# Optimization experiments

Measured on AMD Instinct MI355X. Metric: run time of the kernel, lower is better.

Reference implementation:

```python
import math
import jax, jax.numpy as jnp
import numpy as np

B, S, DIM = 2, 4096, 512
HEADS, DIM_HEAD, CHUNK = 8, 64, 64
DIM_INNER = HEADS * DIM_HEAD
EPS = 1e-6


def rmsnorm(x, scale):
    var = jnp.mean(x * x, axis=-1, keepdims=True)
    return x * jax.lax.rsqrt(var + EPS) * scale


def mem_attn(p, x):
    # x: [c, dh] single chunk; tiny causal attention memory model
    q = x @ p['wq']
    k = x @ p['wk']
    v = x @ p['wv1']
    d = q.shape[-1]
    dots = (q @ k.T) * (d ** -0.5)
    c = x.shape[-2]
    mask = jnp.tril(jnp.ones((c, c), dtype=bool))
    dots = jnp.where(mask, dots, -1e9)
    attn = jax.nn.softmax(dots, axis=-1)
    hidden = attn @ v
    return jax.nn.silu(hidden) @ p['wv2']


def mem_loss(p, inp, tgt):
    pred = mem_attn(p, inp)
    return jnp.sum(jnp.mean((pred - tgt) ** 2, axis=-1))


def assoc_scan(gates, vals):
    # first-order linear recurrence y_t = g_t * y_{t-1} + v_t along axis=1
    def op(a, b):
        a1, b1 = a
        a2, b2 = b
        return a1 * a2, a2 * b1 + b2
    return jax.lax.associative_scan(op, (gates, vals), axis=1)


def setup_inputs():
    key = jax.random.key(0)
    ks = jax.random.split(key, 16)
    n = lambda k, shp, s: jax.random.normal(k, shp, dtype=jnp.float32) * s
    return {
        'seq': n(ks[0], (B, S, DIM), 1.0),
        'w_store_norm': jnp.ones((DIM,), jnp.float32),
        'w_retrieve_norm': jnp.ones((DIM,), jnp.float32),
        'w_post_norm': jnp.ones((DIM,), jnp.float32),
        'w_q': n(ks[1], (DIM, DIM_INNER), DIM ** -0.5),
        'w_kv': n(ks[2], (DIM, 2 * DIM_INNER), DIM ** -0.5),
        'w_step': n(ks[3], (DIM, HEADS), DIM ** -0.5),
        'w_mom': n(ks[4], (DIM, HEADS), DIM ** -0.5),
        'w_decay': n(ks[5], (DIM, HEADS), DIM ** -0.5),
        'w_combine': n(ks[6], (DIM_INNER, DIM), DIM_INNER ** -0.5),
        'wq': n(ks[7], (DIM_HEAD, DIM_HEAD), 0.01),
        'wk': n(ks[8], (DIM_HEAD, DIM_HEAD), 0.01),
        'wv1': n(ks[9], (DIM_HEAD, DIM_HEAD), 0.01),
        'wv2': n(ks[10], (DIM_HEAD, DIM_HEAD), 0.01),
    }


def reference(seq, w_store_norm, w_retrieve_norm, w_post_norm, w_q, w_kv,
              w_step, w_mom, w_decay, w_combine, wq, wk, wv1, wv2):
    b, s_len, d = seq.shape
    c, h, dh = CHUNK, HEADS, DIM_HEAD
    past = {'wq': wq, 'wk': wk, 'wv1': wv1, 'wv2': wv2}

    # ---------- store_memories ----------
    s = rmsnorm(seq, w_store_norm)
    n_full = (s_len // c) * c
    s = s[:, :n_full]
    nc = n_full // c

    # adaptive lr: [b,n,h] -> (b h) n -> chunk-mean [bh, nc]
    lr = jnp.exp(jax.nn.sigmoid(s @ w_step) * -15.0)
    lr = jnp.transpose(lr, (0, 2, 1)).reshape(b * h, nc, c).mean(-1)

    s_mean = s.reshape(b, nc, c, d).mean(2)  # [b, nc, d]
    mom_gate = jax.nn.sigmoid(s_mean @ w_mom)
    mom_gate = jnp.transpose(mom_gate, (0, 2, 1)).reshape(b * h, nc, 1)
    decay = jax.nn.sigmoid(s_mean @ w_decay)
    decay = jnp.transpose(decay, (0, 2, 1)).reshape(b * h, nc, 1)

    keys, values = jnp.split(s @ w_kv, 2, axis=-1)

    def chunkify(t):  # [b, n, h*dh] -> [(b h nc), c, dh]
        t = t.reshape(b, n_full, h, dh)
        t = jnp.transpose(t, (0, 2, 1, 3))
        return t.reshape(b * h * nc, c, dh)

    keys, values = chunkify(keys), chunkify(values)

    # per-chunk meta-gradients wrt shared memory-model params
    grads = jax.vmap(jax.grad(mem_loss), in_axes=(None, 0, 0))(past, keys, values)

    updates = {}
    for name in past:
        g = grads[name].reshape(b * h, nc, dh * dh)
        surprise = g * (-lr)[..., None]
        _, momentum = assoc_scan(mom_gate, surprise)
        _, upd = assoc_scan(1.0 - decay, momentum)
        updates[name] = upd.reshape(b * h, nc, dh, dh)

    wwu = {k2: past[k2][None, None] + updates[k2] for k2 in past}  # [bh, nc, dh, dh]

    # ---------- retrieve_memories ----------
    r = rmsnorm(seq, w_retrieve_norm)
    rc = r[:, c:]
    curtailed = s_len - c
    next_len = ((curtailed + 1 + c - 1) // c) * c
    pad = next_len - curtailed
    rc = jnp.pad(rc, ((0, 0), (0, pad), (0, 0)))

    q = rc @ w_q  # [b, next_len, h*dh]
    q = q.reshape(b, next_len, h, dh)
    q = jnp.transpose(q, (0, 2, 1, 3)).reshape(b * h * (next_len // c), c, dh)

    pc = {k2: v2.reshape(b * h * nc, dh, dh) for k2, v2 in wwu.items()}
    vals = jax.vmap(mem_attn)(pc, q)  # [(bh nc), c, dh]
    vals = vals.reshape(b, h, next_len, dh)
    vals = jnp.transpose(vals, (0, 2, 1, 3)).reshape(b, next_len, h * dh)
    vals = rmsnorm(vals @ w_combine, w_post_norm)
    vals = jnp.pad(vals, ((0, 0), (c, 0), (0, 0)))
    return vals[:, :-pad]
```

## Files before the change

kernel.cpp:

```cpp
#include <hip/hip_runtime.h>
#include <math.h>

constexpr int BATCH = 2, SEQ = 4096, DIM = 512, HEADS = 8, DH = 64, CH = 64;
constexpr int NC = SEQ / CH;
constexpr int BH = BATCH * HEADS;
constexpr int NCHUNK = BH * NC;
constexpr int ROWS = BATCH * SEQ;
constexpr int DI = HEADS * DH;
constexpr int TS = 64 * 72;

typedef __attribute__((ext_vector_type(8))) short short8;
typedef __attribute__((ext_vector_type(4))) short short4v;
typedef __attribute__((ext_vector_type(4))) float f32x4;

__device__ inline float sigmoidf_(float x){ return 1.f/(1.f+__expf(-x)); }
__device__ inline float dsilu_f(float x){ float s = sigmoidf_(x); return s*(1.f + x*(1.f-s)); }

__device__ inline unsigned short f2b(float f){
  union { float f; unsigned int u; } c; c.f = f;
  unsigned int u = c.u;
  unsigned int r = (u + 0x7FFFu + ((u >> 16) & 1u)) >> 16;
  return (unsigned short)r;
}
__device__ inline float b2f(unsigned short h){
  union { unsigned int u; float f; } c; c.u = ((unsigned int)h) << 16;
  return c.f;
}

struct MM { int lr, lg, rowbase, colbase; };
__device__ inline MM mmctx(){
  int tid = threadIdx.x;
  int wid = tid >> 6, lane = tid & 63;
  MM m; m.lr = lane & 15; m.lg = lane >> 4;
  m.rowbase = (wid >> 1) * 16; m.colbase = (wid & 1) * 32;
  return m;
}

template<bool SILUA>
__device__ inline void mm64(const unsigned short* A, const unsigned short* B,
                            f32x4 (&acc)[2], const MM& m)
{
  acc[0] = (f32x4){0.f,0.f,0.f,0.f};
  acc[1] = (f32x4){0.f,0.f,0.f,0.f};
  #pragma unroll
  for (int ks = 0; ks < 2; ks++){
    short8 a = *(const short8*)&A[(m.rowbase + m.lr)*72 + ks*32 + m.lg*8];
    if constexpr (SILUA){
      #pragma unroll
      for (int j = 0; j < 8; j++){
        float v = b2f((unsigned short)a[j]);
        v = v * sigmoidf_(v);
        a[j] = (short)f2b(v);
      }
    }
    #pragma unroll
    for (int ct = 0; ct < 2; ct++){
      short8 b = *(const short8*)&B[(m.colbase + ct*16 + m.lr)*72 + ks*32 + m.lg*8];
      acc[ct] = __builtin_amdgcn_mfma_f32_16x16x32_bf16(a, b, acc[ct], 0, 0, 0);
    }
  }
}

__device__ inline void storeN64(unsigned short* R, const f32x4 (&acc)[2], const MM& m, float scale){
  #pragma unroll
  for (int ct = 0; ct < 2; ct++){
    int c  = m.colbase + ct*16 + m.lr;
    int mb = m.rowbase + m.lg*4;
    #pragma unroll
    for (int r = 0; r < 4; r++) R[(mb+r)*72 + c] = f2b(acc[ct][r] * scale);
  }
}
__device__ inline void storeT64(unsigned short* T, const f32x4 (&acc)[2], const MM& m, float scale){
  #pragma unroll
  for (int ct = 0; ct < 2; ct++){
    int c  = m.colbase + ct*16 + m.lr;
    int mb = m.rowbase + m.lg*4;
    short4v p;
    #pragma unroll
    for (int r = 0; r < 4; r++) p[r] = (short)f2b(acc[ct][r] * scale);
    *(short4v*)&T[c*72 + mb] = p;
  }
}
__device__ inline void storeSC(float* S, const f32x4 (&acc)[2], const MM& m, float scale){
  #pragma unroll
  for (int ct = 0; ct < 2; ct++){
    int c  = m.colbase + ct*16 + m.lr;
    int mb = m.rowbase + m.lg*4;
    #pragma unroll
    for (int r = 0; r < 4; r++) S[(mb+r)*66 + c] = acc[ct][r] * scale;
  }
}
__device__ inline void storeGTb64(unsigned short* __restrict__ G, const f32x4 (&acc)[2],
                                  const MM& m, float scale){
  #pragma unroll
  for (int ct = 0; ct < 2; ct++){
    int c  = m.colbase + ct*16 + m.lr;
    int mb = m.rowbase + m.lg*4;
    short4v p;
    #pragma unroll
    for (int r = 0; r < 4; r++) p[r] = (short)f2b(acc[ct][r] * scale);
    *(short4v*)&G[c*64 + mb] = p;
  }
}

__device__ inline void loadTileBrow(unsigned short* R, const unsigned short* __restrict__ src,
                                    int stride, int tid){
  int i = tid >> 3, j8 = (tid & 7) * 8;
  *(short8*)&R[i*72 + j8] = *(const short8*)&src[(size_t)i*stride + j8];
}
__device__ inline void loadTileBrowT(unsigned short* R, unsigned short* T,
                                     const unsigned short* __restrict__ src,
                                     int stride, int tid){
  int i = tid >> 3, j8 = (tid & 7) * 8;
  short8 v = *(const short8*)&src[(size_t)i*stride + j8];
  *(short8*)&R[i*72 + j8] = v;
  #pragma unroll
  for (int jj = 0; jj < 8; jj++) T[(j8+jj)*72 + i] = (unsigned short)v[jj];
}

__global__ __launch_bounds__(256) void k_front(
    const float* __restrict__ seq, const float* __restrict__ wsn,
    const float* __restrict__ wrn, const float* __restrict__ wstep,
    const float* __restrict__ w_kv, const float* __restrict__ w_q,
    const float* __restrict__ wcomb,
    const float* __restrict__ wq, const float* __restrict__ wk,
    const float* __restrict__ wv1, const float* __restrict__ wv2,
    unsigned short* __restrict__ s_hi, unsigned short* __restrict__ s_lo,
    unsigned short* __restrict__ rq_hi, float* __restrict__ lrp,
    unsigned short* __restrict__ wkvT_hi, unsigned short* __restrict__ wkvT_lo,
    unsigned short* __restrict__ wqT_hi, unsigned short* __restrict__ wcombT_hi,
    unsigned short* __restrict__ wpre)
{
  __shared__ float t[64][65];
  int tid = threadIdx.x;
  if (blockIdx.x >= ROWS/4){
    int blk = blockIdx.x - ROWS/4;
    if (blk < 256){
      const float* src; unsigned short *dhi, *dlo;
      int R, C, bx, by;
      if (blk < 128){ src = w_kv;  dhi = wkvT_hi;  dlo = wkvT_lo; R = DIM; C = 2*DI; bx = blk & 15; by = blk >> 4; }
      else if (blk < 192){ int q = blk - 128; src = w_q;   dhi = wqT_hi;    dlo = nullptr; R = DIM; C = DI;  bx = q & 7; by = q >> 3; }
      else               { int q = blk - 192; src = wcomb; dhi = wcombT_hi; dlo = nullptr; R = DI;  C = DIM; bx = q & 7; by = q >> 3; }
      int c0 = bx * 64, r0 = by * 64;
      #pragma unroll
      for (int it = 0; it < 16; it++){
        int idx = it*256 + tid;
        int i = idx >> 6, j = idx & 63;
        t[i][j] = src[(size_t)(r0+i)*C + c0 + j];
      }
      __syncthreads();
      #pragma unroll
      for (int it = 0; it < 16; it++){
        int idx = it*256 + tid;
        int i = idx >> 6, j = idx & 63;
        float v = t[j][i];
        unsigned short hi = f2b(v);
        dhi[(size_t)(c0+i)*R + r0 + j] = hi;
        if (dlo) dlo[(size_t)(c0+i)*R + r0 + j] = f2b(v - b2f(hi));
      }
    } else {
      int b = blk - 256;
      const float* src = (b==0) ? wq : (b==1) ? wk : (b==2) ? wv1 : wv2;
      #pragma unroll
      for (int it = 0; it < 16; it++){
        int idx = it*256 + tid;
        int i = idx >> 6, j = idx & 63;
        t[i][j] = src[i*64 + j];
      }
      __syncthreads();
      #pragma unroll
      for (int it = 0; it < 16; it++){
        int idx = it*256 + tid;
        int i = idx >> 6, j = idx & 63;
        wpre[b*4096 + i*64 + j] = f2b(t[j][i]);
        if (b == 3) wpre[4*4096 + i*64 + j] = f2b(t[i][j]);
      }
    }
    return;
  }
  int wid = tid >> 6, lane = tid & 63;
  int row = blockIdx.x * 4 + wid;
  int b = row >> 12, tt = row & 4095;
  const float* x = seq + (size_t)row * DIM;
  float4 v0 = *(const float4*)&x[lane*4];
  float4 v1 = *(const float4*)&x[256 + lane*4];
  float xv[8] = {v0.x, v0.y, v0.z, v0.w, v1.x, v1.y, v1.z, v1.w};
  float ss = 0.f;
  #pragma unroll
  for (int j = 0; j < 8; j++) ss += xv[j]*xv[j];
  #pragma unroll
  for (int m = 1; m < 64; m <<= 1) ss += __shfl_xor(ss, m);
  float rinv = rsqrtf(ss * (1.f/DIM) + 1e-6f);

  float4 w0 = *(const float4*)&wsn[lane*4];
  float4 w1 = *(const float4*)&wsn[256 + lane*4];
  float wv[8] = {w0.x, w0.y, w0.z, w0.w, w1.x, w1.y, w1.z, w1.w};
  float sv[8];
  short4v h0, h1, l0, l1;
  #pragma unroll
  for (int j = 0; j < 8; j++){
    sv[j] = xv[j] * rinv * wv[j];
    unsigned short hi = f2b(sv[j]);
    unsigned short lo = f2b(sv[j] - b2f(hi));
    if (j < 4){ h0[j] = (short)hi; l0[j] = (short)lo; }
    else      { h1[j-4] = (short)hi; l1[j-4] = (short)lo; }
  }
  size_t sbase = (size_t)row*DIM + lane*4;
  *(short4v*)&s_hi[sbase] = h0; *(short4v*)&s_hi[sbase + 256] = h1;
  *(short4v*)&s_lo[sbase] = l0; *(short4v*)&s_lo[sbase + 256] = l1;

  if (tt >= CH){
    float4 r0 = *(const float4*)&wrn[lane*4];
    float4 r1 = *(const float4*)&wrn[256 + lane*4];
    float rv[8] = {r0.x, r0.y, r0.z, r0.w, r1.x, r1.y, r1.z, r1.w};
    short4v rh0, rh1;
    #pragma unroll
    for (int j = 0; j < 8; j++){
      float q = xv[j] * rinv * rv[j];
      unsigned short hi = f2b(q);
      if (j < 4) rh0[j] = (short)hi; else rh1[j-4] = (short)hi;
    }
    size_t rbase = ((size_t)b*SEQ + (tt - CH))*DIM + lane*4;
    *(short4v*)&rq_hi[rbase] = rh0; *(short4v*)&rq_hi[rbase + 256] = rh1;
  } else {
    short4v z; z[0]=0; z[1]=0; z[2]=0; z[3]=0;
    size_t rbase = ((size_t)b*SEQ + (SEQ - CH + tt))*DIM + lane*4;
    *(short4v*)&rq_hi[rbase] = z; *(short4v*)&rq_hi[rbase + 256] = z;
  }

  float acc[8] = {0.f,0.f,0.f,0.f,0.f,0.f,0.f,0.f};
  #pragma unroll
  for (int j = 0; j < 8; j++){
    int e = (j < 4) ? (lane*4 + j) : (256 + lane*4 + (j-4));
    float4 wa = *(const float4*)&wstep[e*8];
    float4 wb = *(const float4*)&wstep[e*8 + 4];
    acc[0] += sv[j]*wa.x; acc[1] += sv[j]*wa.y; acc[2] += sv[j]*wa.z; acc[3] += sv[j]*wa.w;
    acc[4] += sv[j]*wb.x; acc[5] += sv[j]*wb.y; acc[6] += sv[j]*wb.z; acc[7] += sv[j]*wb.w;
  }
  #pragma unroll
  for (int m = 1; m < 64; m <<= 1){
    #pragma unroll
    for (int h = 0; h < 8; h++) acc[h] += __shfl_xor(acc[h], m);
  }
  float a = acc[0];
  #pragma unroll
  for (int h = 1; h < 8; h++) a = (lane == h) ? acc[h] : a;
  if (lane < 8)
    lrp[(size_t)row*HEADS + lane] = __expf(-15.f * sigmoidf_(a));
}

__global__ __launch_bounds__(256, 2) void k_mid(
    const unsigned short* __restrict__ s_hi, const unsigned short* __restrict__ s_lo,
    const unsigned short* __restrict__ rq_hi,
    const unsigned short* __restrict__ wkvT_hi, const unsigned short* __restrict__ wkvT_lo,
    const unsigned short* __restrict__ wqT_hi,
    unsigned short* __restrict__ kvb, unsigned short* __restrict__ qb,
    float* __restrict__ kvv,
    const float* __restrict__ lrp, const float* __restrict__ wmom,
    const float* __restrict__ wdec,
    float* __restrict__ mg, float* __restrict__ dec, float* __restrict__ lrc)
{
  __shared__ __align__(16) unsigned short AhS[128*72];
  __shared__ __align__(16) unsigned short BhS[128*72];
  __shared__ __align__(16) unsigned short AlS[128*72];
  __shared__ __align__(16) unsigned short BlS[128*72];
  int tid = threadIdx.x;
  int z = blockIdx.z;
  if (z == 3){
    int bid = blockIdx.y * gridDim.x + blockIdx.x;
    if (bid >= BATCH*NC) return;
    float* smean = (float*)AhS;
    int b = bid >> 6, ch = bid & 63;
    size_t off = ((size_t)(b*SEQ + ch*CH)) * DIM;
    for (int e = tid; e < DIM; e += 256){
      float acc = 0.f;
      for (int i = 0; i < CH; i++)
        acc += b2f(s_hi[off + (size_t)i*DIM + e]);
      smean[e] = acc * (1.f/CH);
    }
    __syncthreads();
    int gh = tid >> 5, l = tid & 31;
    float am = 0.f, ad = 0.f;
    for (int e = l; e < DIM; e += 32){
      float v = smean[e];
      am += v * wmom[e*HEADS + gh];
      ad += v * wdec[e*HEADS + gh];
    }
    const float* lrbase = lrp + ((size_t)(b*SEQ + ch*CH)) * HEADS + gh;
    float al = lrbase[(size_t)l*HEADS] + lrbase[(size_t)(l+32)*HEADS];
    #pragma unroll
    for (int m = 1; m < 32; m <<= 1){
      am += __shfl_xor(am, m);
      ad += __shfl_xor(ad, m);
      al += __shfl_xor(al, m);
    }
    if (l == 0){
      int o = (b*HEADS + gh)*NC + ch;
      mg[o]  = sigmoidf_(am);
      dec[o] = sigmoidf_(ad);
      lrc[o] = al * (1.f/CH);
    }
    return;
  }
  const bool LO = (z == 2);
  const unsigned short* Ahg = (z == 1) ? rq_hi : s_hi;
  const unsigned short* Alg = s_lo;
  const unsigned short* Bhg = (z == 0) ? wkvT_hi : (z == 1) ? wqT_hi
                                       : wkvT_hi + (size_t)DI*DIM;
  const unsigned short* Blg = wkvT_lo + (size_t)DI*DIM;
  const int M = ROWS, N = DI, K = DIM;

  int nwg = gridDim.x * gridDim.y;
  int bid = blockIdx.y * gridDim.x + blockIdx.x;
  int swz = (bid & 7) * (nwg >> 3) + (bid >> 3);
  int m0 = (swz / gridDim.x) * 128;
  int n0 = (swz % gridDim.x) * 128;
  int wid = tid >> 6, lane = tid & 63;
  int lr = lane & 15, lg = lane >> 4;
  int wr = (wid >> 1) * 64, wc = (wid & 1) * 64;
  f32x4 acc[4][4];
  #pragma unroll
  for (int r = 0; r < 4; r++)
    #pragma unroll
    for (int c = 0; c < 4; c++) acc[r][c] = (f32x4){0.f,0.f,0.f,0.f};

  for (int k0 = 0; k0 < K; k0 += 64){
    #pragma unroll
    for (int it = 0; it < 4; it++){
      int idx = it*256 + tid;
      int row = idx >> 3, col8 = (idx & 7) * 8;
      size_t ga = (size_t)(m0+row)*K + k0 + col8;
      size_t gb = (size_t)(n0+row)*K + k0 + col8;
      *(short8*)&AhS[row*72 + col8] = *(const short8*)&Ahg[ga];
      *(short8*)&BhS[row*72 + col8] = *(const short8*)&Bhg[gb];
      if (LO){
        *(short8*)&AlS[row*72 + col8] = *(const short8*)&Alg[ga];
        *(short8*)&BlS[row*72 + col8] = *(const short8*)&Blg[gb];
      }
    }
    __syncthreads();
    #pragma unroll
    for (int ks = 0; ks < 2; ks++){
      short8 ah[4], al[4], bh[4], bl[4];
      #pragma unroll
      for (int i = 0; i < 4; i++){
        int ao = (wr + i*16 + lr)*72 + ks*32 + lg*8;
        int bo = (wc + i*16 + lr)*72 + ks*32 + lg*8;
        ah[i] = *(const short8*)&AhS[ao];
        bh[i] = *(const short8*)&BhS[bo];
        if (LO){
          al[i] = *(const short8*)&AlS[ao];
          bl[i] = *(const short8*)&BlS[bo];
        }
      }
      #pragma unroll
      for (int r = 0; r < 4; r++)
        #pragma unroll
        for (int c = 0; c < 4; c++){
          acc[r][c] = __builtin_amdgcn_mfma_f32_16x16x32_bf16(ah[r], bh[c], acc[r][c], 0, 0, 0);
          if (LO){
            acc[r][c] = __builtin_amdgcn_mfma_f32_16x16x32_bf16(ah[r], bl[c], acc[r][c], 0, 0, 0);
            acc[r][c] = __builtin_amdgcn_mfma_f32_16x16x32_bf16(al[r], bh[c], acc[r][c], 0, 0, 0);
          }
        }
    }
    __syncthreads();
  }
  unsigned short* Cb = (z == 1) ? qb : kvb;
  #pragma unroll
  for (int rt = 0; rt < 4; rt++)
    #pragma unroll
    for (int ct = 0; ct < 4; ct++){
      int col = n0 + wc + ct*16 + lr;
      int rowb = m0 + wr + rt*16 + lg*4;
      #pragma unroll
      for (int r = 0; r < 4; r++){
        float v = acc[rt][ct][r];
        if (LO) kvv[(size_t)(rowb+r)*N + col] = v;
        else    Cb[(size_t)(rowb+r)*N + col] = f2b(v);
      }
    }
}

__global__ __launch_bounds__(256, 4) void k_gemm1(
    const unsigned short* __restrict__ Ahg, const unsigned short* __restrict__ Bhg,
    unsigned short* __restrict__ Cb, int M, int N, int K)
{
  __shared__ __align__(16) unsigned short AhS[128*72];
  __shared__ __align__(16) unsigned short BhS[128*72];
  int tid = threadIdx.x;
  int nwg = gridDim.x * gridDim.y;
  int bid = blockIdx.y * gridDim.x + blockIdx.x;
  int swz = (bid & 7) * (nwg >> 3) + (bid >> 3);
  int m0 = (swz / gridDim.x) * 128;
  int n0 = (swz % gridDim.x) * 128;
  int wid = tid >> 6, lane = tid & 63;
  int lr = lane & 15, lg = lane >> 4;
  int wr = (wid >> 1) * 64, wc = (wid & 1) * 64;
  f32x4 acc[4][4];
  #pragma unroll
  for (int r = 0; r < 4; r++)
    #pragma unroll
    for (int c = 0; c < 4; c++) acc[r][c] = (f32x4){0.f,0.f,0.f,0.f};

  for (int k0 = 0; k0 < K; k0 += 64){
    #pragma unroll
    for (int it = 0; it < 4; it++){
      int idx = it*256 + tid;
      int row = idx >> 3, col8 = (idx & 7) * 8;
      *(short8*)&AhS[row*72 + col8] = *(const short8*)&Ahg[(size_t)(m0+row)*K + k0 + col8];
      *(short8*)&BhS[row*72 + col8] = *(const short8*)&Bhg[(size_t)(n0+row)*K + k0 + col8];
    }
    __syncthreads();
    #pragma unroll
    for (int ks = 0; ks < 2; ks++){
      short8 ah[4], bh[4];
      #pragma unroll
      for (int i = 0; i < 4; i++){
        ah[i] = *(const short8*)&AhS[(wr + i*16 + lr)*72 + ks*32 + lg*8];
        bh[i] = *(const short8*)&BhS[(wc + i*16 + lr)*72 + ks*32 + lg*8];
      }
      #pragma unroll
      for (int r = 0; r < 4; r++)
        #pragma unroll
        for (int c = 0; c < 4; c++)
          acc[r][c] = __builtin_amdgcn_mfma_f32_16x16x32_bf16(ah[r], bh[c], acc[r][c], 0, 0, 0);
    }
    __syncthreads();
  }
  #pragma unroll
  for (int rt = 0; rt < 4; rt++)
    #pragma unroll
    for (int ct = 0; ct < 4; ct++){
      int col = n0 + wc + ct*16 + lr;
      int rowb = m0 + wr + rt*16 + lg*4;
      #pragma unroll
      for (int r = 0; r < 4; r++)
        Cb[(size_t)(rowb+r)*N + col] = f2b(acc[rt][ct][r]);
    }
}

__global__ __launch_bounds__(512) void k_grads(
    const unsigned short* __restrict__ kvb, const float* __restrict__ kvv,
    const unsigned short* __restrict__ wpre,
    const float* __restrict__ lrc, unsigned short* __restrict__ g)
{
  __shared__ __align__(16) unsigned short sm[12*TS];
  __shared__ __align__(16) float SC[64*66];
  unsigned short *Xr = sm,        *XT = sm + TS,
                 *s2 = sm + 2*TS, *s3 = sm + 3*TS, *s4 = sm + 4*TS,
                 *s5 = sm + 5*TS, *s6 = sm + 6*TS, *s7 = sm + 7*TS,
                 *s8 = sm + 8*TS, *s9 = sm + 9*TS, *s10 = sm + 10*TS,
                 *s11 = sm + 11*TS;
  unsigned short *SCu = (unsigned short*)SC;
  int chunk = blockIdx.x;
  int bh = chunk >> 6, t = chunk & 63;
  int b = bh >> 3, h = bh & 7;
  int tid = threadIdx.x;
  MM M = mmctx();
  const unsigned short* xb = kvb + ((size_t)(b*SEQ + t*CH)) * DI + h*DH;
  const float* tbase = kvv + ((size_t)(b*SEQ + t*CH)) * DI + h*DH;
  float negLr = -lrc[bh*NC + t];
  f32x4 acc[2], accV[2];

  loadTileBrowT(Xr, XT, xb, DI, tid);
  loadTileBrow(s2, wpre + 0*4096, 64, tid);
  loadTileBrow(s3, wpre + 1*4096, 64, tid);
  loadTileBrow(s4, wpre + 2*4096, 64, tid);
  loadTileBrow(s5, wpre + 3*4096, 64, tid);
  loadTileBrow(s6, wpre + 4*4096, 64, tid);
  __syncthreads();
  mm64<false>(Xr, s2, acc, M);
  storeN64(s7, acc, M, 1.f); storeT64(s8, acc, M, 1.f);
  mm64<false>(Xr, s3, acc, M);
  storeN64(s9, acc, M, 1.f); storeT64(s10, acc, M, 1.f);
  mm64<false>(Xr, s4, accV, M);
  storeN64(s11, accV, M, 1.f);
  __syncthreads();
  storeT64(s2, accV, M, 1.f);
  mm64<false>(s7, s9, acc, M);
  storeSC(SC, acc, M, 0.125f);
  __syncthreads();
  {
    int row = tid >> 3, q = tid & 7;
    float p[8];
    float mx = -1e30f;
    #pragma unroll
    for (int cc = 0; cc < 8; cc++){
      int col = q*8 + cc;
      float x = SC[row*66 + col];
      p[cc] = (col <= row) ? x : -1e9f;
      mx = fmaxf(mx, p[cc]);
    }
    mx = fmaxf(mx, __shfl_xor(mx, 1));
    mx = fmaxf(mx, __shfl_xor(mx, 2));
    mx = fmaxf(mx, __shfl_xor(mx, 4));
    float sum = 0.f;
    #pragma unroll
    for (int cc = 0; cc < 8; cc++){ p[cc] = __expf(p[cc] - mx); sum += p[cc]; }
    sum += __shfl_xor(sum, 1);
    sum += __shfl_xor(sum, 2);
    sum += __shfl_xor(sum, 4);
    float inv = 1.f / sum;
    #pragma unroll
    for (int cc = 0; cc < 8; cc++){
      int col = q*8 + cc;
      unsigned short hh = f2b(p[cc] * inv);
      s7[row*72 + col] = hh;
      s9[col*72 + row] = hh;
    }
  }
  __syncthreads();
  mm64<false>(s7, s2, acc, M);
  storeN64(s3, acc, M, 1.f); storeT64(s4, acc, M, 1.f);
  __syncthreads();
  mm64<true>(s3, s5, acc, M);
  #pragma unroll
  for (int ct = 0; ct < 2; ct++){
    int c  = M.colbase + ct*16 + M.lr;
    int mb = M.rowbase + M.lg*4;
    #pragma unroll
    for (int r = 0; r < 4; r++){
      float t2 = (acc[ct][r] - tbase[(size_t)(mb+r)*DI + c]) * (2.f/64.f);
      unsigned short hh = f2b(t2);
      Xr[(mb+r)*72 + c] = hh;
      s2[c*72 + (mb+r)] = hh;
    }
  }
  __syncthreads();
  mm64<true>(s4, s2, acc, M);
  storeGTb64(g + ((size_t)(3*NCHUNK + chunk))*4096, acc, M, negLr);
  mm64<false>(Xr, s6, acc, M);
  #pragma unroll
  for (int ct = 0; ct < 2; ct++){
    int c  = M.colbase + ct*16 + M.lr;
    int mb = M.rowbase + M.lg*4;
    #pragma unroll
    for (int r = 0; r < 4; r++){
      float x = b2f(s3[(mb+r)*72 + c]);
      float d = acc[ct][r] * dsilu_f(x);
      unsigned short hh = f2b(d);
      s5[(mb+r)*72 + c] = hh;
      SCu[c*72 + (mb+r)] = hh;
    }
  }
  __syncthreads();
  mm64<false>(s5, s11, acc, M);
  storeN64(Xr, acc, M, 1.f);
  mm64<false>(s9, SCu, acc, M);
  storeT64(s2, acc, M, 1.f);
  __syncthreads();
  {
    int row = tid >> 3, q = tid & 7;
    float da[8], a[8], rs = 0.f;
    #pragma unroll
    for (int cc = 0; cc < 8; cc++){
      int col = q*8 + cc;
      da[cc] = b2f(Xr[row*72 + col]);
      a[cc]  = b2f(s7[row*72 + col]);
      rs += da[cc]*a[cc];
    }
    rs += __shfl_xor(rs, 1);
    rs += __shfl_xor(rs, 2);
    rs += __shfl_xor(rs, 4);
    #pragma unroll
    for (int cc = 0; cc < 8; cc++){
      int col = q*8 + cc;
      unsigned short hh = f2b(a[cc] * (da[cc] - rs));
      s3[row*72 + col] = hh;
      s6[col*72 + row] = hh;
    }
  }
  mm64<false>(XT, s2, acc, M);
  storeGTb64(g + ((size_t)(2*NCHUNK + chunk))*4096, acc, M, negLr);
  __syncthreads();
  mm64<false>(s3, s10, acc, M);
  storeT64(Xr, acc, M, 0.125f);
  mm64<false>(s6, s8, acc, M);
  storeT64(s2, acc, M, 0.125f);
  __syncthreads();
  mm64<false>(XT, Xr, acc, M);
  storeGTb64(g + ((size_t)(0*NCHUNK + chunk))*4096, acc, M, negLr);
  mm64<false>(XT, s2, acc, M);
  storeGTb64(g + ((size_t)(1*NCHUNK + chunk))*4096, acc, M, negLr);
}

__global__ __launch_bounds__(256) void k_scan(
    unsigned short* __restrict__ g, const float* __restrict__ mg, const float* __restrict__ dec,
    const float* __restrict__ wq, const float* __restrict__ wk,
    const float* __restrict__ wv1, const float* __restrict__ wv2)
{
  int idx = blockIdx.x * 256 + threadIdx.x;
  int e = (idx & 2047) * 2;
  int bh = (idx >> 11) & 15;
  int name = idx >> 15;
  const float* past = (name == 0) ? wq : (name == 1) ? wk : (name == 2) ? wv1 : wv2;
  float base0 = past[(e & 63)*64 + (e >> 6)];
  float base1 = past[((e+1) & 63)*64 + ((e+1) >> 6)];
  const float* mgb = mg + bh*NC;
  const float* dcb = dec + bh*NC;
  size_t baseoff = ((size_t)name*NCHUNK + (size_t)bh*NC)*4096 + e;
  float m0 = 0.f, u0 = 0.f, m1 = 0.f, u1 = 0.f;
  for (int t = 0; t < NC; t++){
    size_t off = baseoff + (size_t)t*4096;
    unsigned int v = *(const unsigned int*)&g[off];
    float su0 = b2f((unsigned short)(v & 0xffff));
    float su1 = b2f((unsigned short)(v >> 16));
    float gm = mgb[t], dc = dcb[t];
    m0 = gm*m0 + su0;  u0 = (1.f - dc)*u0 + m0;
    m1 = gm*m1 + su1;  u1 = (1.f - dc)*u1 + m1;
    unsigned int w = (unsigned int)f2b(base0 + u0) | ((unsigned int)f2b(base1 + u1) << 16);
    *(unsigned int*)&g[off] = w;
  }
}

__global__ __launch_bounds__(512, 4) void k_retrieve(
    const unsigned short* __restrict__ qb, const unsigned short* __restrict__ Wg,
    unsigned short* __restrict__ vals_hi)
{
  __shared__ __align__(16) unsigned short sm[6*TS];
  __shared__ __align__(16) float SC[64*66];
  unsigned short *Xr = sm,       *Wt = sm + TS,   *Qr = sm + 2*TS,
                 *Kr = sm + 3*TS, *Vt = sm + 4*TS, *Hr = sm + 5*TS;
  unsigned short *Ar = (unsigned short*)SC;
  int chunk = blockIdx.x;
  int bh = chunk >> 6, t = chunk & 63;
  int b = bh >> 3, h = bh & 7;
  int tid = threadIdx.x;
  MM M = mmctx();
  const unsigned short* xb = qb + ((size_t)(b*SEQ + t*CH)) * DI + h*DH;
  f32x4 acc[2], accV[2];

  loadTileBrow(Xr, xb, DI, tid);
  loadTileBrow(Wt, Wg + ((size_t)(0*NCHUNK + chunk))*4096, 64, tid);
  __syncthreads();
  mm64<false>(Xr, Wt, acc, M); storeN64(Qr, acc, M, 1.f);
  loadTileBrow(Hr, Wg + ((size_t)(1*NCHUNK + chunk))*4096, 64, tid);
  __syncthreads();
  mm64<false>(Xr, Hr, acc, M); storeN64(Kr, acc, M, 1.f);
  loadTileBrow(Wt, Wg + ((size_t)(2*NCHUNK + chunk))*4096, 64, tid);
  __syncthreads();
  mm64<false>(Xr, Wt, accV, M); storeT64(Vt, accV, M, 1.f);
  mm64<false>(Qr, Kr, acc, M); storeSC(SC, acc, M, 0.125f);
  loadTileBrow(Hr, Wg + ((size_t)(3*NCHUNK + chunk))*4096, 64, tid);
  __syncthreads();
  {
    int row = tid >> 3, q = tid & 7;
    float p[8];
    float mx = -1e30f;
    #pragma unroll
    for (int cc = 0; cc < 8; cc++){
      int col = q*8 + cc;
      float x = SC[row*66 + col];
      p[cc] = (col <= row) ? x : -1e9f;
      mx = fmaxf(mx, p[cc]);
    }
    mx = fmaxf(mx, __shfl_xor(mx, 1));
    mx = fmaxf(mx, __shfl_xor(mx, 2));
    mx = fmaxf(mx, __shfl_xor(mx, 4));
    float sum = 0.f;
    #pragma unroll
    for (int cc = 0; cc < 8; cc++){ p[cc] = __expf(p[cc] - mx); sum += p[cc]; }
    sum += __shfl_xor(sum, 1);
    sum += __shfl_xor(sum, 2);
    sum += __shfl_xor(sum, 4);
    float inv = 1.f / sum;
    __syncthreads();
    #pragma unroll
    for (int cc = 0; cc < 8; cc++){
      int col = q*8 + cc;
      Ar[row*72 + col] = f2b(p[cc] * inv);
    }
  }
  __syncthreads();
  mm64<false>(Ar, Vt, acc, M); storeN64(Kr, acc, M, 1.f);
  __syncthreads();
  mm64<true>(Kr, Hr, acc, M);
  #pragma unroll
  for (int ct = 0; ct < 2; ct++){
    int c  = M.colbase + ct*16 + M.lr;
    int mb = M.rowbase + M.lg*4;
    #pragma unroll
    for (int r = 0; r < 4; r++){
      size_t o = ((size_t)(b*SEQ + t*CH + mb + r))*DI + h*DH + c;
      vals_hi[o] = f2b(acc[ct][r]);
    }
  }
}

__global__ __launch_bounds__(256) void k_outnorm(
    const unsigned short* __restrict__ tmp, const float* __restrict__ wpn,
    float* __restrict__ out)
{
  int wid = threadIdx.x >> 6, lane = threadIdx.x & 63;
  int row = blockIdx.x * 4 + wid;
  int b = row >> 12, r = row & 4095;
  float* dst = out + ((size_t)b*SEQ + r) * DIM;
  if (r < CH){
    float4 z = make_float4(0.f, 0.f, 0.f, 0.f);
    *(float4*)&dst[lane*8] = z;
    *(float4*)&dst[lane*8 + 4] = z;
    return;
  }
  const unsigned short* src = tmp + ((size_t)b*SEQ + (r - CH)) * DIM;
  short8 t0 = *(const short8*)&src[lane*8];
  float xv[8];
  #pragma unroll
  for (int j = 0; j < 8; j++) xv[j] = b2f((unsigned short)t0[j]);
  float ss = 0.f;
  #pragma unroll
  for (int j = 0; j < 8; j++) ss += xv[j]*xv[j];
  #pragma unroll
  for (int m = 1; m < 64; m <<= 1) ss += __shfl_xor(ss, m);
  float rinv = rsqrtf(ss * (1.f/DIM) + 1e-6f);
  float4 o0, o1;
  o0.x = xv[0]*rinv*wpn[lane*8+0]; o0.y = xv[1]*rinv*wpn[lane*8+1];
  o0.z = xv[2]*rinv*wpn[lane*8+2]; o0.w = xv[3]*rinv*wpn[lane*8+3];
  o1.x = xv[4]*rinv*wpn[lane*8+4]; o1.y = xv[5]*rinv*wpn[lane*8+5];
  o1.z = xv[6]*rinv*wpn[lane*8+6]; o1.w = xv[7]*rinv*wpn[lane*8+7];
  *(float4*)&dst[lane*8] = o0;
  *(float4*)&dst[lane*8 + 4] = o1;
}

extern "C" void kernel_launch(void* const* d_in, const int* in_sizes, int n_in,
                              void* d_out, int out_size, void* d_ws, size_t ws_size,
                              hipStream_t stream)
{
  (void)in_sizes; (void)n_in; (void)ws_size; (void)out_size;
  const float* seq   = (const float*)d_in[0];
  const float* wsn   = (const float*)d_in[1];
  const float* wrn   = (const float*)d_in[2];
  const float* wpn   = (const float*)d_in[3];
  const float* w_q   = (const float*)d_in[4];
  const float* w_kv  = (const float*)d_in[5];
  const float* wstep = (const float*)d_in[6];
  const float* wmom  = (const float*)d_in[7];
  const float* wdec  = (const float*)d_in[8];
  const float* wcomb = (const float*)d_in[9];
  const float* wq    = (const float*)d_in[10];
  const float* wk    = (const float*)d_in[11];
  const float* wv1   = (const float*)d_in[12];
  const float* wv2   = (const float*)d_in[13];
  float* out = (float*)d_out;

  char* p = (char*)d_ws;
  unsigned short* s_hi  = (unsigned short*)p; p += (size_t)ROWS*DIM*2;
  unsigned short* s_lo  = (unsigned short*)p; p += (size_t)ROWS*DIM*2;
  unsigned short* rq_hi = (unsigned short*)p; p += (size_t)ROWS*DIM*2;
  unsigned short* kvb   = (unsigned short*)p; p += (size_t)ROWS*DI*2;
  float* kvv            = (float*)p;          p += (size_t)ROWS*DI*4;
  unsigned short* qb    = (unsigned short*)p; p += (size_t)ROWS*DI*2;
  unsigned short* g     = (unsigned short*)p; p += (size_t)4*NCHUNK*4096*2;
  float* lrp            = (float*)p;          p += (size_t)ROWS*HEADS*4;
  float* mg             = (float*)p;          p += (size_t)BH*NC*4;
  float* dec            = (float*)p;          p += (size_t)BH*NC*4;
  float* lrc            = (float*)p;          p += (size_t)BH*NC*4;
  unsigned short* wkvT_hi   = (unsigned short*)p; p += (size_t)(2*DI)*DIM*2;
  unsigned short* wkvT_lo   = (unsigned short*)p; p += (size_t)(2*DI)*DIM*2;
  unsigned short* wqT_hi    = (unsigned short*)p; p += (size_t)DI*DIM*2;
  unsigned short* wcombT_hi = (unsigned short*)p; p += (size_t)DIM*DI*2;
  unsigned short* wpre      = (unsigned short*)p; p += (size_t)5*4096*2;
  unsigned short* vals_hi   = (unsigned short*)p; p += (size_t)ROWS*DI*2;
  unsigned short* tmp = s_hi;

  k_front<<<ROWS/4 + 260, 256, 0, stream>>>(
      seq, wsn, wrn, wstep, w_kv, w_q, wcomb, wq, wk, wv1, wv2,
      s_hi, s_lo, rq_hi, lrp, wkvT_hi, wkvT_lo, wqT_hi, wcombT_hi, wpre);
  k_mid<<<dim3(DI/128, ROWS/128, 4), 256, 0, stream>>>(
      s_hi, s_lo, rq_hi, wkvT_hi, wkvT_lo, wqT_hi,
      kvb, qb, kvv, lrp, wmom, wdec, mg, dec, lrc);
  k_grads<<<NCHUNK, 512, 0, stream>>>(kvb, kvv, wpre, lrc, g);
  k_scan<<<(4*BH*2048)/256, 256, 0, stream>>>(g, mg, dec, wq, wk, wv1, wv2);
  k_retrieve<<<NCHUNK, 512, 0, stream>>>(qb, g, vals_hi);
  k_gemm1<<<dim3(DIM/128, ROWS/128), 256, 0, stream>>>(
      vals_hi, wcombT_hi, tmp, ROWS, DIM, DI);
  k_outnorm<<<ROWS/4, 256, 0, stream>>>(tmp, wpn, out);
}
```

Before: 174.4 us.

## Drop split-bf16 value projection, fuse kv GEMM into single bf16 pass

Removes the hi/lo bf16 split used to compute the value projection with near-fp32 accuracy. The value half of kv is now produced in plain bf16 inside one wider GEMM (N=2*DI) together with the key half, and stored as bf16 instead of fp32. This eliminates the 3x MFMA work and extra loads for the lo path, the fp32 kvv buffer, and the lo tensors written by the front kernel. The launch grid is flattened to 896 blocks and occupancy is raised to 4 blocks per CU. The cost is lower precision in the value target used in the gradient computation.

```diff
diff --git a/kernel.cpp b/kernel.cpp
--- a/kernel.cpp
+++ b/kernel.cpp
@@ -125,9 +125,9 @@
     const float* __restrict__ wcomb,
     const float* __restrict__ wq, const float* __restrict__ wk,
     const float* __restrict__ wv1, const float* __restrict__ wv2,
-    unsigned short* __restrict__ s_hi, unsigned short* __restrict__ s_lo,
+    unsigned short* __restrict__ s_hi,
     unsigned short* __restrict__ rq_hi, float* __restrict__ lrp,
-    unsigned short* __restrict__ wkvT_hi, unsigned short* __restrict__ wkvT_lo,
+    unsigned short* __restrict__ wkvT_hi,
     unsigned short* __restrict__ wqT_hi, unsigned short* __restrict__ wcombT_hi,
     unsigned short* __restrict__ wpre)
 {
@@ -136,11 +136,11 @@
   if (blockIdx.x >= ROWS/4){
     int blk = blockIdx.x - ROWS/4;
     if (blk < 256){
-      const float* src; unsigned short *dhi, *dlo;
+      const float* src; unsigned short *dhi;
       int R, C, bx, by;
-      if (blk < 128){ src = w_kv;  dhi = wkvT_hi;  dlo = wkvT_lo; R = DIM; C = 2*DI; bx = blk & 15; by = blk >> 4; }
-      else if (blk < 192){ int q = blk - 128; src = w_q;   dhi = wqT_hi;    dlo = nullptr; R = DIM; C = DI;  bx = q & 7; by = q >> 3; }
-      else               { int q = blk - 192; src = wcomb; dhi = wcombT_hi; dlo = nullptr; R = DI;  C = DIM; bx = q & 7; by = q >> 3; }
+      if (blk < 128){ src = w_kv;  dhi = wkvT_hi;  R = DIM; C = 2*DI; bx = blk & 15; by = blk >> 4; }
+      else if (blk < 192){ int q = blk - 128; src = w_q;   dhi = wqT_hi;    R = DIM; C = DI;  bx = q & 7; by = q >> 3; }
+      else               { int q = blk - 192; src = wcomb; dhi = wcombT_hi; R = DI;  C = DIM; bx = q & 7; by = q >> 3; }
       int c0 = bx * 64, r0 = by * 64;
       #pragma unroll
       for (int it = 0; it < 16; it++){
@@ -153,10 +153,7 @@
       for (int it = 0; it < 16; it++){
         int idx = it*256 + tid;
         int i = idx >> 6, j = idx & 63;
-        float v = t[j][i];
-        unsigned short hi = f2b(v);
-        dhi[(size_t)(c0+i)*R + r0 + j] = hi;
-        if (dlo) dlo[(size_t)(c0+i)*R + r0 + j] = f2b(v - b2f(hi));
+        dhi[(size_t)(c0+i)*R + r0 + j] = f2b(t[j][i]);
       }
     } else {
       int b = blk - 256;
@@ -196,18 +193,15 @@
   float4 w1 = *(const float4*)&wsn[256 + lane*4];
   float wv[8] = {w0.x, w0.y, w0.z, w0.w, w1.x, w1.y, w1.z, w1.w};
   float sv[8];
-  short4v h0, h1, l0, l1;
+  short4v h0, h1;
   #pragma unroll
   for (int j = 0; j < 8; j++){
     sv[j] = xv[j] * rinv * wv[j];
     unsigned short hi = f2b(sv[j]);
-    unsigned short lo = f2b(sv[j] - b2f(hi));
-    if (j < 4){ h0[j] = (short)hi; l0[j] = (short)lo; }
-    else      { h1[j-4] = (short)hi; l1[j-4] = (short)lo; }
+    if (j < 4) h0[j] = (short)hi; else h1[j-4] = (short)hi;
   }
   size_t sbase = (size_t)row*DIM + lane*4;
   *(short4v*)&s_hi[sbase] = h0; *(short4v*)&s_hi[sbase + 256] = h1;
-  *(short4v*)&s_lo[sbase] = l0; *(short4v*)&s_lo[sbase + 256] = l1;
 
   if (tt >= CH){
     float4 r0 = *(const float4*)&wrn[lane*4];
@@ -249,26 +243,20 @@
     lrp[(size_t)row*HEADS + lane] = __expf(-15.f * sigmoidf_(a));
 }
 
-__global__ __launch_bounds__(256, 2) void k_mid(
-    const unsigned short* __restrict__ s_hi, const unsigned short* __restrict__ s_lo,
-    const unsigned short* __restrict__ rq_hi,
-    const unsigned short* __restrict__ wkvT_hi, const unsigned short* __restrict__ wkvT_lo,
-    const unsigned short* __restrict__ wqT_hi,
+__global__ __launch_bounds__(256, 4) void k_mid(
+    const unsigned short* __restrict__ s_hi, const unsigned short* __restrict__ rq_hi,
+    const unsigned short* __restrict__ wkvT_hi, const unsigned short* __restrict__ wqT_hi,
     unsigned short* __restrict__ kvb, unsigned short* __restrict__ qb,
-    float* __restrict__ kvv,
     const float* __restrict__ lrp, const float* __restrict__ wmom,
     const float* __restrict__ wdec,
     float* __restrict__ mg, float* __restrict__ dec, float* __restrict__ lrc)
 {
   __shared__ __align__(16) unsigned short AhS[128*72];
   __shared__ __align__(16) unsigned short BhS[128*72];
-  __shared__ __align__(16) unsigned short AlS[128*72];
-  __shared__ __align__(16) unsigned short BlS[128*72];
   int tid = threadIdx.x;
-  int z = blockIdx.z;
-  if (z == 3){
-    int bid = blockIdx.y * gridDim.x + blockIdx.x;
-    if (bid >= BATCH*NC) return;
+  int blk = blockIdx.x;
+  if (blk >= 768){
+    int bid = blk - 768;
     float* smean = (float*)AhS;
     int b = bid >> 6, ch = bid & 63;
     size_t off = ((size_t)(b*SEQ + ch*CH)) * DIM;
@@ -302,19 +290,15 @@
     }
     return;
   }
-  const bool LO = (z == 2);
-  const unsigned short* Ahg = (z == 1) ? rq_hi : s_hi;
-  const unsigned short* Alg = s_lo;
-  const unsigned short* Bhg = (z == 0) ? wkvT_hi : (z == 1) ? wqT_hi
-                                       : wkvT_hi + (size_t)DI*DIM;
-  const unsigned short* Blg = wkvT_lo + (size_t)DI*DIM;
-  const int M = ROWS, N = DI, K = DIM;
-
-  int nwg = gridDim.x * gridDim.y;
-  int bid = blockIdx.y * gridDim.x + blockIdx.x;
+  const unsigned short *Ahg, *Bhg; unsigned short* Cb;
+  int N, nwg, bid;
+  if (blk < 512){ Ahg = s_hi;  Bhg = wkvT_hi; Cb = kvb; N = 2*DI; nwg = 512; bid = blk; }
+  else          { Ahg = rq_hi; Bhg = wqT_hi;  Cb = qb;  N = DI;   nwg = 256; bid = blk - 512; }
+  const int K = DIM;
+  int ntil = N >> 7;
   int swz = (bid & 7) * (nwg >> 3) + (bid >> 3);
-  int m0 = (swz / gridDim.x) * 128;
-  int n0 = (swz % gridDim.x) * 128;
+  int m0 = (swz / ntil) * 128;
+  int n0 = (swz % ntil) * 128;
   int wid = tid >> 6, lane = tid & 63;
   int lr = lane & 15, lg = lane >> 4;
   int wr = (wid >> 1) * 64, wc = (wid & 1) * 64;
@@ -329,44 +313,26 @@
     for (int it = 0; it < 4; it++){
       int idx = it*256 + tid;
       int row = idx >> 3, col8 = (idx & 7) * 8;
-      size_t ga = (size_t)(m0+row)*K + k0 + col8;
-      size_t gb = (size_t)(n0+row)*K + k0 + col8;
-      *(short8*)&AhS[row*72 + col8] = *(const short8*)&Ahg[ga];
-      *(short8*)&BhS[row*72 + col8] = *(const short8*)&Bhg[gb];
-      if (LO){
-        *(short8*)&AlS[row*72 + col8] = *(const short8*)&Alg[ga];
-        *(short8*)&BlS[row*72 + col8] = *(const short8*)&Blg[gb];
-      }
+      *(short8*)&AhS[row*72 + col8] = *(const short8*)&Ahg[(size_t)(m0+row)*K + k0 + col8];
+      *(short8*)&BhS[row*72 + col8] = *(const short8*)&Bhg[(size_t)(n0+row)*K + k0 + col8];
     }
     __syncthreads();
     #pragma unroll
     for (int ks = 0; ks < 2; ks++){
-      short8 ah[4], al[4], bh[4], bl[4];
+      short8 ah[4], bh[4];
       #pragma unroll
       for (int i = 0; i < 4; i++){
-        int ao = (wr + i*16 + lr)*72 + ks*32 + lg*8;
-        int bo = (wc + i*16 + lr)*72 + ks*32 + lg*8;
-        ah[i] = *(const short8*)&AhS[ao];
-        bh[i] = *(const short8*)&BhS[bo];
-        if (LO){
-          al[i] = *(const short8*)&AlS[ao];
-          bl[i] = *(const short8*)&BlS[bo];
-        }
+        ah[i] = *(const short8*)&AhS[(wr + i*16 + lr)*72 + ks*32 + lg*8];
+        bh[i] = *(const short8*)&BhS[(wc + i*16 + lr)*72 + ks*32 + lg*8];
       }
       #pragma unroll
       for (int r = 0; r < 4; r++)
         #pragma unroll
-        for (int c = 0; c < 4; c++){
+        for (int c = 0; c < 4; c++)
           acc[r][c] = __builtin_amdgcn_mfma_f32_16x16x32_bf16(ah[r], bh[c], acc[r][c], 0, 0, 0);
-          if (LO){
-            acc[r][c] = __builtin_amdgcn_mfma_f32_16x16x32_bf16(ah[r], bl[c], acc[r][c], 0, 0, 0);
-            acc[r][c] = __builtin_amdgcn_mfma_f32_16x16x32_bf16(al[r], bh[c], acc[r][c], 0, 0, 0);
-          }
-        }
     }
     __syncthreads();
   }
-  unsigned short* Cb = (z == 1) ? qb : kvb;
   #pragma unroll
   for (int rt = 0; rt < 4; rt++)
     #pragma unroll
@@ -374,11 +340,8 @@
       int col = n0 + wc + ct*16 + lr;
       int rowb = m0 + wr + rt*16 + lg*4;
       #pragma unroll
-      for (int r = 0; r < 4; r++){
-        float v = acc[rt][ct][r];
-        if (LO) kvv[(size_t)(rowb+r)*N + col] = v;
-        else    Cb[(size_t)(rowb+r)*N + col] = f2b(v);
-      }
+      for (int r = 0; r < 4; r++)
+        Cb[(size_t)(rowb+r)*N + col] = f2b(acc[rt][ct][r]);
     }
 }
 
@@ -441,7 +404,7 @@
 }
 
 __global__ __launch_bounds__(512) void k_grads(
-    const unsigned short* __restrict__ kvb, const float* __restrict__ kvv,
+    const unsigned short* __restrict__ kvb,
     const unsigned short* __restrict__ wpre,
     const float* __restrict__ lrc, unsigned short* __restrict__ g)
 {
@@ -458,12 +421,12 @@
   int b = bh >> 3, h = bh & 7;
   int tid = threadIdx.x;
   MM M = mmctx();
-  const unsigned short* xb = kvb + ((size_t)(b*SEQ + t*CH)) * DI + h*DH;
-  const float* tbase = kvv + ((size_t)(b*SEQ + t*CH)) * DI + h*DH;
+  const unsigned short* xb = kvb + ((size_t)(b*SEQ + t*CH)) * (2*DI) + h*DH;
+  const unsigned short* tb = xb + DI;
   float negLr = -lrc[bh*NC + t];
   f32x4 acc[2], accV[2];
 
-  loadTileBrowT(Xr, XT, xb, DI, tid);
+  loadTileBrowT(Xr, XT, xb, 2*DI, tid);
   loadTileBrow(s2, wpre + 0*4096, 64, tid);
   loadTileBrow(s3, wpre + 1*4096, 64, tid);
   loadTileBrow(s4, wpre + 2*4096, 64, tid);
@@ -521,7 +484,7 @@
     int mb = M.rowbase + M.lg*4;
     #pragma unroll
     for (int r = 0; r < 4; r++){
-      float t2 = (acc[ct][r] - tbase[(size_t)(mb+r)*DI + c]) * (2.f/64.f);
+      float t2 = (acc[ct][r] - b2f(tb[(size_t)(mb+r)*(2*DI) + c])) * (2.f/64.f);
       unsigned short hh = f2b(t2);
       Xr[(mb+r)*72 + c] = hh;
       s2[c*72 + (mb+r)] = hh;
@@ -745,10 +708,8 @@
 
   char* p = (char*)d_ws;
   unsigned short* s_hi  = (unsigned short*)p; p += (size_t)ROWS*DIM*2;
-  unsigned short* s_lo  = (unsigned short*)p; p += (size_t)ROWS*DIM*2;
   unsigned short* rq_hi = (unsigned short*)p; p += (size_t)ROWS*DIM*2;
-  unsigned short* kvb   = (unsigned short*)p; p += (size_t)ROWS*DI*2;
-  float* kvv            = (float*)p;          p += (size_t)ROWS*DI*4;
+  unsigned short* kvb   = (unsigned short*)p; p += (size_t)ROWS*2*DI*2;
   unsigned short* qb    = (unsigned short*)p; p += (size_t)ROWS*DI*2;
   unsigned short* g     = (unsigned short*)p; p += (size_t)4*NCHUNK*4096*2;
   float* lrp            = (float*)p;          p += (size_t)ROWS*HEADS*4;
@@ -756,7 +717,6 @@
   float* dec            = (float*)p;          p += (size_t)BH*NC*4;
   float* lrc            = (float*)p;          p += (size_t)BH*NC*4;
   unsigned short* wkvT_hi   = (unsigned short*)p; p += (size_t)(2*DI)*DIM*2;
-  unsigned short* wkvT_lo   = (unsigned short*)p; p += (size_t)(2*DI)*DIM*2;
   unsigned short* wqT_hi    = (unsigned short*)p; p += (size_t)DI*DIM*2;
   unsigned short* wcombT_hi = (unsigned short*)p; p += (size_t)DIM*DI*2;
   unsigned short* wpre      = (unsigned short*)p; p += (size_t)5*4096*2;
@@ -765,11 +725,11 @@
 
   k_front<<<ROWS/4 + 260, 256, 0, stream>>>(
       seq, wsn, wrn, wstep, w_kv, w_q, wcomb, wq, wk, wv1, wv2,
-      s_hi, s_lo, rq_hi, lrp, wkvT_hi, wkvT_lo, wqT_hi, wcombT_hi, wpre);
-  k_mid<<<dim3(DI/128, ROWS/128, 4), 256, 0, stream>>>(
-      s_hi, s_lo, rq_hi, wkvT_hi, wkvT_lo, wqT_hi,
-      kvb, qb, kvv, lrp, wmom, wdec, mg, dec, lrc);
-  k_grads<<<NCHUNK, 512, 0, stream>>>(kvb, kvv, wpre, lrc, g);
+      s_hi, rq_hi, lrp, wkvT_hi, wqT_hi, wcombT_hi, wpre);
+  k_mid<<<896, 256, 0, stream>>>(
+      s_hi, rq_hi, wkvT_hi, wqT_hi, kvb, qb,
+      lrp, wmom, wdec, mg, dec, lrc);
+  k_grads<<<NCHUNK, 512, 0, stream>>>(kvb, wpre, lrc, g);
   k_scan<<<(4*BH*2048)/256, 256, 0, stream>>>(g, mg, dec, wq, wk, wv1, wv2);
   k_retrieve<<<NCHUNK, 512, 0, stream>>>(qb, g, vals_hi);
   k_gemm1<<<dim3(DIM/128, ROWS/128), 256, 0, stream>>>(
```

Result: faster. 152.2 us (median of 2 runs) (-12.7%).
